# Kernel optimization log

Measured on AMD Instinct MI355X. Metric: run time of the kernel, lower is better.

Reference implementation:

```python
import jax, jax.numpy as jnp
import numpy as np

NUM_HEADS = 16
D_MODEL = 1024
MASK_VALUE = -1000000.0


def setup_inputs() -> dict:
    key = jax.random.key(0)
    ks = jax.random.split(key, 8)
    B, S, D = 2, 2048, D_MODEL
    scale = 1.0 / np.sqrt(D)
    return {
        "queries": jax.random.normal(ks[0], (B, S, D), dtype=jnp.float32),
        "keys": jax.random.normal(ks[1], (B, S, D), dtype=jnp.float32),
        "values": jax.random.normal(ks[2], (B, S, D), dtype=jnp.float32),
        "valid_lens": jax.random.randint(ks[3], (B,), 1, S + 1),
        # Linear weights stored as (in, out); no bias (bias=False)
        "Wq": jax.random.normal(ks[4], (D, D), dtype=jnp.float32) * scale,
        "Wk": jax.random.normal(ks[5], (D, D), dtype=jnp.float32) * scale,
        "Wv": jax.random.normal(ks[6], (D, D), dtype=jnp.float32) * scale,
        "Wo": jax.random.normal(ks[7], (D, D), dtype=jnp.float32) * scale,
    }


def reference(queries, keys, values, valid_lens, Wq, Wk, Wv, Wo):
    B, Sq, D = queries.shape
    Sk = keys.shape[1]
    H = NUM_HEADS
    hd = D // H

    def split_heads(x, S):
        # (B, S, D) -> (B, H, S, hd)
        return x.reshape(B, S, H, hd).transpose(0, 2, 1, 3)

    q = split_heads(queries @ Wq, Sq)
    k = split_heads(keys @ Wk, Sk)
    v = split_heads(values @ Wv, Sk)

    # Faithful to original bug: d_k = queries.size(0) after head-flattening = B*H
    scale = 1.0 / jnp.sqrt(jnp.float32(B * H))
    scores = jnp.einsum("bhqd,bhkd->bhqk", q, k) * scale  # (B,H,Sq,Sk)

    # sequence_mask over last dim, per batch row (valid_lens repeated per head)
    mask = jnp.arange(Sk)[None, None, None, :] < valid_lens[:, None, None, None]
    scores = jnp.where(mask, scores, MASK_VALUE)
    attn = jax.nn.softmax(scores, axis=-1)

    out = jnp.einsum("bhqk,bhkd->bhqd", attn, v)  # (B,H,Sq,hd)
    out = out.transpose(0, 2, 1, 3).reshape(B, Sq, D)
    return out @ Wo
```

## Files before the change

kernel.cpp:

```cpp
#include <hip/hip_runtime.h>
#include <stdint.h>

#define NH 16
#define SEQ 2048
#define DMODEL 1024
#define HD 64
#define NBATCH 2
#define MTOT (NBATCH * SEQ)
#define QSCALE 0.17677669529663687f
#define LOG2E 1.4426950408889634f

typedef __bf16 bf16x8 __attribute__((ext_vector_type(8)));
typedef float f32x4 __attribute__((ext_vector_type(4)));
typedef float f32x16 __attribute__((ext_vector_type(16)));
typedef unsigned uint4v __attribute__((ext_vector_type(4)));

__device__ __forceinline__ unsigned short bf16u(float x) {
  unsigned u = __builtin_bit_cast(unsigned, x);
  u += 0x7fffu + ((u >> 16) & 1u);
  return (unsigned short)(u >> 16);
}

__device__ __forceinline__ float exp2_fast(float x) {
  float r;
  asm("v_exp_f32 %0, %1" : "=v"(r) : "v"(x));
  return r;
}

__device__ __forceinline__ f32x4 mfma16(bf16x8 a, bf16x8 b, f32x4 c) {
  return __builtin_amdgcn_mfma_f32_16x16x32_bf16(a, b, c, 0, 0, 0);
}
__device__ __forceinline__ f32x16 mfma32(bf16x8 a, bf16x8 b, f32x16 c) {
  return __builtin_amdgcn_mfma_f32_32x32x16_bf16(a, b, c, 0, 0, 0);
}

__device__ __forceinline__ void gl16(const void* g, void* l) {
  __builtin_amdgcn_global_load_lds(
      (const __attribute__((address_space(1))) void*)g,
      (__attribute__((address_space(3))) void*)l, 16, 0, 0);
}

__device__ __forceinline__ unsigned cvtpk(float a, float b) {
  unsigned r;
  asm("v_cvt_pk_bf16_f32 %0, %1, %2" : "=v"(r) : "v"(a), "v"(b));
  return r;
}


__global__ __launch_bounds__(256) void cast_x_kernel(
    const float* __restrict__ x0, const float* __restrict__ x1,
    const float* __restrict__ x2, unsigned short* __restrict__ o0,
    unsigned short* __restrict__ o1, unsigned short* __restrict__ o2) {
  const float* src = (blockIdx.y == 0) ? x0 : (blockIdx.y == 1) ? x1 : x2;
  unsigned short* dst = (blockIdx.y == 0) ? o0 : (blockIdx.y == 1) ? o1 : o2;
  const int n4 = MTOT * DMODEL / 4;
  for (int i = blockIdx.x * blockDim.x + threadIdx.x; i < n4;
       i += gridDim.x * blockDim.x) {
    float4 f = reinterpret_cast<const float4*>(src)[i];
    ushort4 u;
    u.x = bf16u(f.x); u.y = bf16u(f.y); u.z = bf16u(f.z); u.w = bf16u(f.w);
    reinterpret_cast<ushort4*>(dst)[i] = u;
  }
}

__global__ __launch_bounds__(256) void transpose_w_kernel(
    const float* __restrict__ w0, const float* __restrict__ w1,
    const float* __restrict__ w2, const float* __restrict__ w3,
    unsigned short* __restrict__ t0, unsigned short* __restrict__ t1,
    unsigned short* __restrict__ t2, unsigned short* __restrict__ t3) {
  __shared__ float tile[64][65];
  const float* w = (blockIdx.z == 0) ? w0 : (blockIdx.z == 1) ? w1
                   : (blockIdx.z == 2) ? w2 : w3;
  unsigned short* t = (blockIdx.z == 0) ? t0 : (blockIdx.z == 1) ? t1
                      : (blockIdx.z == 2) ? t2 : t3;
  const float scl = (blockIdx.z == 0) ? QSCALE * LOG2E : 1.0f;
  int k0 = blockIdx.y * 64, n0 = blockIdx.x * 64;
  int tx = threadIdx.x & 63, ty = threadIdx.x >> 6;
#pragma unroll
  for (int i = 0; i < 16; ++i) {
    int kk = ty * 16 + i;
    tile[kk][tx] = w[(k0 + kk) * DMODEL + n0 + tx];
  }
  __syncthreads();
#pragma unroll
  for (int i = 0; i < 16; ++i) {
    int nn = ty * 16 + i;
    t[(n0 + nn) * DMODEL + k0 + tx] = bf16u(tile[tx][nn] * scl);
  }
}

__global__ __launch_bounds__(256) void gemm_qkv_kernel(
    const unsigned short* __restrict__ xq, const unsigned short* __restrict__ xk,
    const unsigned short* __restrict__ xv,
    const unsigned short* __restrict__ wq, const unsigned short* __restrict__ wk,
    const unsigned short* __restrict__ wv,
    unsigned short* __restrict__ qb, unsigned short* __restrict__ kb,
    unsigned short* __restrict__ vb) {
  __shared__ unsigned short lA[2][128 * 32];
  __shared__ unsigned short lB[2][128 * 32];
  const int z = blockIdx.z;
  const unsigned short* A = (z == 0) ? xq : (z == 1) ? xk : xv;
  const unsigned short* Wt = (z == 0) ? wq : (z == 1) ? wk : wv;
  unsigned short* outb = (z == 0) ? qb : (z == 1) ? kb : vb;

  const int tid = threadIdx.x;
  const int lane = tid & 63, wid = tid >> 6;
  const int wr = wid >> 1, wc = wid & 1;
  const int m0 = blockIdx.x * 128, n0 = blockIdx.y * 128;
  const int lm = lane & 15, lg = lane >> 4;
  const int lk = lg * 8;

  auto stage = [&](int buf, int kt) {
#pragma unroll
    for (int i = 0; i < 2; ++i) {
      int c = tid + i * 256;
      int row = c >> 2, cb = c & 3;
      gl16(A + (m0 + row) * DMODEL + kt * 32 + cb * 8, (char*)lA[buf] + c * 16);
      gl16(Wt + (n0 + row) * DMODEL + kt * 32 + cb * 8, (char*)lB[buf] + c * 16);
    }
  };

  f32x4 acc[4][4] = {};
  stage(0, 0);
  __syncthreads();
  int cur = 0;

  for (int kt = 0; kt < DMODEL / 32; ++kt) {
    if (kt + 1 < DMODEL / 32) stage(cur ^ 1, kt + 1);

    bf16x8 af[4], bfr[4];
#pragma unroll
    for (int x = 0; x < 4; ++x) {
      af[x] = *reinterpret_cast<const bf16x8*>(&lA[cur][(wr * 64 + x * 16 + lm) * 32 + lk]);
      bfr[x] = *reinterpret_cast<const bf16x8*>(&lB[cur][(wc * 64 + x * 16 + lm) * 32 + lk]);
    }
#pragma unroll
    for (int mi = 0; mi < 4; ++mi)
#pragma unroll
      for (int ni = 0; ni < 4; ++ni)
        acc[mi][ni] = mfma16(af[mi], bfr[ni], acc[mi][ni]);

    if (kt + 1 < DMODEL / 32) { __syncthreads(); cur ^= 1; }
  }

#pragma unroll
  for (int mi = 0; mi < 4; ++mi)
#pragma unroll
    for (int ni = 0; ni < 4; ++ni) {
      int col = n0 + wc * 64 + ni * 16 + lm;
#pragma unroll
      for (int r = 0; r < 4; ++r) {
        int row = m0 + wr * 64 + mi * 16 + lg * 4 + r;
        int b = row >> 11, s = row & (SEQ - 1);
        int h = col >> 6, d = col & (HD - 1);
        outb[(((b * NH + h) * SEQ + s) * HD + d)] = bf16u(acc[mi][ni][r]);
      }
    }
}

__global__ __launch_bounds__(256) void gemm_out_kernel(
    const unsigned short* __restrict__ A, const unsigned short* __restrict__ Wt,
    float* __restrict__ outf) {
  __shared__ unsigned short lA[2][128 * 32];
  __shared__ unsigned short lB[2][64 * 32];
  const int tid = threadIdx.x;
  const int lane = tid & 63, wr = tid >> 6;
  const int m0 = blockIdx.x * 128, n0 = blockIdx.y * 64;
  const int lm = lane & 15, lg = lane >> 4;
  const int lk = lg * 8;

  auto stage = [&](int buf, int kt) {
#pragma unroll
    for (int i = 0; i < 2; ++i) {
      int c = tid + i * 256;
      int row = c >> 2, cb = c & 3;
      gl16(A + (m0 + row) * DMODEL + kt * 32 + cb * 8, (char*)lA[buf] + c * 16);
    }
    int c = tid;
    int row = c >> 2, cb = c & 3;
    gl16(Wt + (n0 + row) * DMODEL + kt * 32 + cb * 8, (char*)lB[buf] + c * 16);
  };

  f32x4 acc[2][4] = {};
  stage(0, 0);
  __syncthreads();
  int cur = 0;

  for (int kt = 0; kt < DMODEL / 32; ++kt) {
    if (kt + 1 < DMODEL / 32) stage(cur ^ 1, kt + 1);

    bf16x8 af[2], bfr[4];
#pragma unroll
    for (int x = 0; x < 2; ++x)
      af[x] = *reinterpret_cast<const bf16x8*>(&lA[cur][(wr * 32 + x * 16 + lm) * 32 + lk]);
#pragma unroll
    for (int x = 0; x < 4; ++x)
      bfr[x] = *reinterpret_cast<const bf16x8*>(&lB[cur][(x * 16 + lm) * 32 + lk]);
#pragma unroll
    for (int mi = 0; mi < 2; ++mi)
#pragma unroll
      for (int ni = 0; ni < 4; ++ni)
        acc[mi][ni] = mfma16(af[mi], bfr[ni], acc[mi][ni]);

    if (kt + 1 < DMODEL / 32) { __syncthreads(); cur ^= 1; }
  }

#pragma unroll
  for (int mi = 0; mi < 2; ++mi)
#pragma unroll
    for (int ni = 0; ni < 4; ++ni) {
      int col = n0 + ni * 16 + lm;
#pragma unroll
      for (int r = 0; r < 4; ++r) {
        int row = m0 + wr * 32 + mi * 16 + lg * 4 + r;
        outf[row * DMODEL + col] = acc[mi][ni][r];
      }
    }
}

__global__ __launch_bounds__(256) void attn11_kernel(
    const unsigned short* __restrict__ qb, const unsigned short* __restrict__ kb,
    const unsigned short* __restrict__ vb, const int* __restrict__ vlens,
    unsigned short* __restrict__ ao) {
  __shared__ char klds[4][8192];
  const int lane = threadIdx.x & 63;
  const int w = threadIdx.x >> 6;
  const int qi = lane & 31, hi = lane >> 5;
  const int wid = blockIdx.x * 4 + w;
  const int bhi = wid & 31;
  const int chunk = wid >> 5;
  const int b = bhi & 1, h = bhi >> 1;
  const int bh = b * NH + h;
  const int s0w = chunk * 32;
  const int vlen = vlens[b];
  const int nkt = (vlen + 63) >> 6;

  const unsigned short* kbase = kb + bh * SEQ * HD;
  const unsigned short* vbase = vb + (size_t)bh * SEQ * HD;

  const unsigned short* qrow = qb + (bh * SEQ + s0w + qi) * HD;
  bf16x8 qf[4];
#pragma unroll
  for (int ks = 0; ks < 4; ++ks)
    qf[ks] = *reinterpret_cast<const bf16x8*>(qrow + ks * 16 + hi * 8);

  f32x16 oacc[2] = {};
  float m = -3e38f, l = 0.f;

  const int srow = lane >> 3;
  const int scol8 = (lane & 7) ^ (srow & 7);
  auto stageK = [&](int kt) {
    int k0 = kt * 64;
    char* dst = &klds[w][0];
#pragma unroll
    for (int i = 0; i < 8; ++i)
      gl16(kbase + (size_t)(k0 + i * 8 + srow) * HD + scol8 * 8,
           dst + i * 1024);
  };

  auto readK = [&](bf16x8* kr) {
    const char* base = &klds[w][0];
#pragma unroll
    for (int kb2 = 0; kb2 < 2; ++kb2)
#pragma unroll
      for (int ks = 0; ks < 4; ++ks) {
        int row = kb2 * 32 + qi;
        int off = row * 128 + ((ks * 32 + hi * 16) ^ ((qi & 7) << 4));
        kr[kb2 * 4 + ks] = *reinterpret_cast<const bf16x8*>(base + off);
      }
  };

  auto body = [&](int t) {
    const int k0 = t * 64;
    const bool lastt = (t == nkt - 1);

    asm volatile("s_waitcnt vmcnt(0)" ::: "memory");
    __builtin_amdgcn_sched_barrier(0);

    bf16x8 kr[8];
    readK(kr);

    f32x16 s0 = {}, s1 = {};
    __builtin_amdgcn_s_setprio(1);
#pragma unroll
    for (int ks = 0; ks < 4; ++ks) s0 = mfma32(kr[ks], qf[ks], s0);
#pragma unroll
    for (int ks = 0; ks < 4; ++ks) s1 = mfma32(kr[4 + ks], qf[ks], s1);
    __builtin_amdgcn_s_setprio(0);

    asm volatile("s_waitcnt lgkmcnt(0)" ::: "memory");
    __builtin_amdgcn_sched_barrier(0);
    if (!lastt) stageK(t + 1);

    bf16x8 vr[8];
#pragma unroll
    for (int db = 0; db < 2; ++db)
#pragma unroll
      for (int f = 0; f < 4; ++f) {
        const unsigned short* vp =
            vbase + (size_t)(k0 + f * 16 + 4 * hi) * HD + db * 32 + qi;
        bf16x8 tv;
#pragma unroll
        for (int j = 0; j < 8; ++j) {
          int koff = ((j & 3) + 8 * (j >> 2)) * HD;
          tv[j] = *reinterpret_cast<const __bf16*>(vp + koff);
        }
        vr[db * 4 + f] = tv;
      }

    if (lastt) {
#pragma unroll
      for (int r = 0; r < 16; ++r) {
        int key = k0 + (r & 3) + 8 * (r >> 2) + 4 * hi;
        if (key >= vlen) s0[r] = -1.4426950e6f;
        if (key + 32 >= vlen) s1[r] = -1.4426950e6f;
      }
    }

    float mx8[8];
#pragma unroll
    for (int i = 0; i < 8; ++i)
      mx8[i] = fmaxf(fmaxf(s0[i], s0[i + 8]), fmaxf(s1[i], s1[i + 8]));
#pragma unroll
    for (int st = 4; st; st >>= 1)
#pragma unroll
      for (int i = 0; i < st; ++i) mx8[i] = fmaxf(mx8[i], mx8[i + st]);
    float mx = fmaxf(mx8[0], __shfl_xor(mx8[0], 32, 64));
    float mn = fmaxf(m, mx);
    float sf = exp2_fast(m - mn);
    m = mn;

#pragma unroll
    for (int r = 0; r < 16; ++r) s0[r] = exp2_fast(s0[r] - mn);
#pragma unroll
    for (int r = 0; r < 16; ++r) s1[r] = exp2_fast(s1[r] - mn);
    float sm8[8];
#pragma unroll
    for (int i = 0; i < 8; ++i)
      sm8[i] = (s0[i] + s0[i + 8]) + (s1[i] + s1[i + 8]);
#pragma unroll
    for (int st = 4; st; st >>= 1)
#pragma unroll
      for (int i = 0; i < st; ++i) sm8[i] += sm8[i + st];
    float ps = sm8[0] + __shfl_xor(sm8[0], 32, 64);
    l = l * sf + ps;
#pragma unroll
    for (int db = 0; db < 2; ++db) oacc[db] *= sf;

    bf16x8 pf[4];
    auto packP = [&](const f32x16& s, bf16x8* out) {
#pragma unroll
      for (int f = 0; f < 2; ++f) {
        uint4v wv;
#pragma unroll
        for (int k2 = 0; k2 < 4; ++k2)
          wv[k2] = cvtpk(s[f * 8 + k2 * 2], s[f * 8 + k2 * 2 + 1]);
        out[f] = __builtin_bit_cast(bf16x8, wv);
      }
    };
    packP(s0, pf);
    packP(s1, pf + 2);

    __builtin_amdgcn_s_setprio(1);
#pragma unroll
    for (int db = 0; db < 2; ++db)
#pragma unroll
      for (int f = 0; f < 4; ++f)
        oacc[db] = mfma32(vr[db * 4 + f], pf[f], oacc[db]);
    __builtin_amdgcn_s_setprio(0);
  };

  stageK(0);
  for (int t = 0; t < nkt; ++t) body(t);

  const float linv = 1.0f / l;
#pragma unroll
  for (int db = 0; db < 2; ++db)
#pragma unroll
    for (int rq = 0; rq < 4; ++rq) {
      ushort4 o;
      o.x = bf16u(oacc[db][rq * 4 + 0] * linv);
      o.y = bf16u(oacc[db][rq * 4 + 1] * linv);
      o.z = bf16u(oacc[db][rq * 4 + 2] * linv);
      o.w = bf16u(oacc[db][rq * 4 + 3] * linv);
      int d = db * 32 + 8 * rq + 4 * hi;
      *reinterpret_cast<ushort4*>(
          ao + (b * SEQ + s0w + qi) * DMODEL + h * HD + d) = o;
    }
}

extern "C" void kernel_launch(void* const* d_in, const int* in_sizes, int n_in,
                              void* d_out, int out_size, void* d_ws, size_t ws_size,
                              hipStream_t stream) {
  (void)in_sizes; (void)n_in; (void)out_size; (void)ws_size;
  const float* q = (const float*)d_in[0];
  const float* k = (const float*)d_in[1];
  const float* v = (const float*)d_in[2];
  const int* vlens = (const int*)d_in[3];
  const float* Wq = (const float*)d_in[4];
  const float* Wk = (const float*)d_in[5];
  const float* Wv = (const float*)d_in[6];
  const float* Wo = (const float*)d_in[7];
  float* out = (float*)d_out;

  char* ws = (char*)d_ws;
  const size_t MB = 1u << 20;
  unsigned short* xq = (unsigned short*)(ws + 0 * MB);
  unsigned short* xk = (unsigned short*)(ws + 8 * MB);
  unsigned short* xv = (unsigned short*)(ws + 16 * MB);
  unsigned short* wqt = (unsigned short*)(ws + 24 * MB);
  unsigned short* wkt = (unsigned short*)(ws + 26 * MB);
  unsigned short* wvt = (unsigned short*)(ws + 28 * MB);
  unsigned short* wot = (unsigned short*)(ws + 30 * MB);
  unsigned short* qb = (unsigned short*)(ws + 32 * MB);
  unsigned short* kb = (unsigned short*)(ws + 40 * MB);
  unsigned short* vb = (unsigned short*)(ws + 48 * MB);
  unsigned short* ao = (unsigned short*)(ws + 56 * MB);

  cast_x_kernel<<<dim3(512, 3), 256, 0, stream>>>(q, k, v, xq, xk, xv);
  transpose_w_kernel<<<dim3(16, 16, 4), 256, 0, stream>>>(Wq, Wk, Wv, Wo,
                                                          wqt, wkt, wvt, wot);
  gemm_qkv_kernel<<<dim3(32, 8, 3), 256, 0, stream>>>(xq, xk, xv, wqt, wkt, wvt,
                                                      qb, kb, vb);
  attn11_kernel<<<dim3(512), 256, 0, stream>>>(qb, kb, vb, vlens, ao);
  gemm_out_kernel<<<dim3(32, 16), 256, 0, stream>>>(ao, wot, out);
}
```

Measured before the change: 123.3 us.

## Split attention key range across wave pairs and merge partial softmax states

Each 32-query tile is now processed by two waves that each handle half of the key tiles, doubling the grid to 1024 blocks. Partial outputs and their running max and sum are exchanged through LDS, combined with a log-sum-exp rescale, and each wave writes half of the head dimension. This is meant to raise parallelism and shorten the per-wave serial key loop, which matters for long valid lengths. The cost is extra LDS traffic, a block-wide barrier, and the merge arithmetic at the end.

Measured after the change: 146.0 us. 1.18x slower.

```diff
diff --git a/kernel.cpp b/kernel.cpp
--- a/kernel.cpp
+++ b/kernel.cpp
@@ -218,22 +218,27 @@
     }
 }
 
-__global__ __launch_bounds__(256) void attn11_kernel(
+__global__ __launch_bounds__(256) void attn12_kernel(
     const unsigned short* __restrict__ qb, const unsigned short* __restrict__ kb,
     const unsigned short* __restrict__ vb, const int* __restrict__ vlens,
     unsigned short* __restrict__ ao) {
   __shared__ char klds[4][8192];
+  __shared__ float sml[4][2][64];
   const int lane = threadIdx.x & 63;
   const int w = threadIdx.x >> 6;
   const int qi = lane & 31, hi = lane >> 5;
-  const int wid = blockIdx.x * 4 + w;
-  const int bhi = wid & 31;
-  const int chunk = wid >> 5;
+  const int half = w & 1;
+  const int p = blockIdx.x * 2 + (w >> 1);
+  const int bhi = p & 31;
+  const int chunk = p >> 5;
   const int b = bhi & 1, h = bhi >> 1;
   const int bh = b * NH + h;
   const int s0w = chunk * 32;
   const int vlen = vlens[b];
   const int nkt = (vlen + 63) >> 6;
+  const int nkt2 = (nkt + 1) >> 1;
+  const int tstart = half ? nkt2 : 0;
+  const int tend = half ? nkt : nkt2;
 
   const unsigned short* kbase = kb + bh * SEQ * HD;
   const unsigned short* vbase = vb + (size_t)bh * SEQ * HD;
@@ -272,7 +277,8 @@
 
   auto body = [&](int t) {
     const int k0 = t * 64;
-    const bool lastt = (t == nkt - 1);
+    const bool lastg = (t == nkt - 1);
+    const bool lastl = (t + 1 >= tend);
 
     asm volatile("s_waitcnt vmcnt(0)" ::: "memory");
     __builtin_amdgcn_sched_barrier(0);
@@ -290,7 +296,7 @@
 
     asm volatile("s_waitcnt lgkmcnt(0)" ::: "memory");
     __builtin_amdgcn_sched_barrier(0);
-    if (!lastt) stageK(t + 1);
+    if (!lastl) stageK(t + 1);
 
     bf16x8 vr[8];
 #pragma unroll
@@ -308,7 +314,7 @@
         vr[db * 4 + f] = tv;
       }
 
-    if (lastt) {
+    if (lastg) {
 #pragma unroll
       for (int r = 0; r < 16; ++r) {
         int key = k0 + (r & 3) + 8 * (r >> 2) + 4 * hi;
@@ -370,23 +376,44 @@
     __builtin_amdgcn_s_setprio(0);
   };
 
-  stageK(0);
-  for (int t = 0; t < nkt; ++t) body(t);
-
-  const float linv = 1.0f / l;
+  if (tstart < tend) stageK(tstart);
+  for (int t = tstart; t < tend; ++t) body(t);
+
+  asm volatile("s_waitcnt vmcnt(0) lgkmcnt(0)" ::: "memory");
+  float* pO = (float*)&klds[w][0];
 #pragma unroll
   for (int db = 0; db < 2; ++db)
 #pragma unroll
-    for (int rq = 0; rq < 4; ++rq) {
-      ushort4 o;
-      o.x = bf16u(oacc[db][rq * 4 + 0] * linv);
-      o.y = bf16u(oacc[db][rq * 4 + 1] * linv);
-      o.z = bf16u(oacc[db][rq * 4 + 2] * linv);
-      o.w = bf16u(oacc[db][rq * 4 + 3] * linv);
-      int d = db * 32 + 8 * rq + 4 * hi;
-      *reinterpret_cast<ushort4*>(
-          ao + (b * SEQ + s0w + qi) * DMODEL + h * HD + d) = o;
-    }
+    for (int r = 0; r < 16; ++r)
+      pO[(db * 16 + r) * 64 + lane] = oacc[db][r];
+  sml[w][0][lane] = m;
+  sml[w][1][lane] = l;
+  __syncthreads();
+
+  const float* qO = (const float*)&klds[w ^ 1][0];
+  const float mB = sml[w ^ 1][0][lane];
+  const float lB = sml[w ^ 1][1][lane];
+  const float mn = fmaxf(m, mB);
+  const float fa = exp2_fast(m - mn), fb = exp2_fast(mB - mn);
+  const float lc = l * fa + lB * fb;
+  const float linv = 1.0f / lc;
+
+  const int db = half;
+#pragma unroll
+  for (int rq = 0; rq < 4; ++rq) {
+    float oc[4];
+#pragma unroll
+    for (int j = 0; j < 4; ++j) {
+      int r = rq * 4 + j;
+      oc[j] = (oacc[db][r] * fa + qO[(db * 16 + r) * 64 + lane] * fb) * linv;
+    }
+    ushort4 o;
+    o.x = bf16u(oc[0]); o.y = bf16u(oc[1]);
+    o.z = bf16u(oc[2]); o.w = bf16u(oc[3]);
+    int d = db * 32 + 8 * rq + 4 * hi;
+    *reinterpret_cast<ushort4*>(
+        ao + (b * SEQ + s0w + qi) * DMODEL + h * HD + d) = o;
+  }
 }
 
 extern "C" void kernel_launch(void* const* d_in, const int* in_sizes, int n_in,
@@ -422,6 +449,6 @@
                                                           wqt, wkt, wvt, wot);
   gemm_qkv_kernel<<<dim3(32, 8, 3), 256, 0, stream>>>(xq, xk, xv, wqt, wkt, wvt,
                                                       qb, kb, vb);
-  attn11_kernel<<<dim3(512), 256, 0, stream>>>(qb, kb, vb, vlens, ao);
+  attn12_kernel<<<dim3(1024), 256, 0, stream>>>(qb, kb, vb, vlens, ao);
   gemm_out_kernel<<<dim3(32, 16), 256, 0, stream>>>(ao, wot, out);
 }
```
